# Kernel tuning notes

Measured on AMD Instinct MI355X. Metric: run time of the kernel, lower is better.

The kernel has to match this reference:

```python
import jax, jax.numpy as jnp
import numpy as np

NUM_HEADS = 16
CAUSAL = True


def setup_inputs() -> dict:
    key = jax.random.key(0)
    ks = jax.random.split(key, 3)
    B, T, D = 2, 2048, 1024
    s = 1.0 / np.sqrt(D)
    return {
        "x": jax.random.normal(ks[0], (B, T, D), dtype=jnp.float32),
        "W_qkv": jax.random.normal(ks[1], (3 * D, D), dtype=jnp.float32) * s,
        "b_qkv": jnp.zeros((3 * D,), dtype=jnp.float32),
        "W_out": jax.random.normal(ks[2], (D, D), dtype=jnp.float32) * s,
        "b_out": jnp.zeros((D,), dtype=jnp.float32),
    }


def reference(x, W_qkv, b_qkv, W_out, b_out):
    B, T, D = x.shape
    H = NUM_HEADS
    hd = D // H
    # qkv projection: torch Linear y = x @ W.T + b
    qkv = jnp.einsum('btd,ed->bte', x, W_qkv) + b_qkv  # [B,T,3D]
    qkv = qkv.reshape(B, T, H, 3 * hd).transpose(0, 2, 1, 3)  # [B,H,T,3hd]
    q, k, v = jnp.split(qkv, 3, axis=-1)  # each [B,H,T,hd]
    scale = 1.0 / np.sqrt(hd).astype(np.float32)
    scores = jnp.einsum('bhtd,bhsd->bhts', q, k) * scale  # [B,H,T,T]
    if CAUSAL:
        mask = jnp.triu(jnp.ones((T, T), dtype=bool), k=1)
        scores = jnp.where(mask, jnp.float32(-jnp.inf), scores)
    weights = jax.nn.softmax(scores, axis=-1)
    attn = jnp.einsum('bhts,bhsd->bhtd', weights, v)  # [B,H,T,hd]
    out = attn.transpose(0, 2, 1, 3).reshape(B, T, D)
    return jnp.einsum('btd,ed->bte', out, W_out) + b_out
```

## Files before the change

### kernel.cpp

```cpp
#include <hip/hip_runtime.h>
#include <hip/hip_bf16.h>
#include <cstdint>


using short8  = __attribute__((ext_vector_type(8))) short;
using floatx4 = __attribute__((ext_vector_type(4))) float;

#define LDS_STRIDE 40

__device__ __forceinline__ float bf16_to_f32(unsigned short u) {
    union { unsigned int i; float f; } v; v.i = ((unsigned int)u) << 16; return v.f;
}
__device__ __forceinline__ unsigned short f32_to_bf16(float f) {
    union { float f; unsigned int i; } v; v.f = f;
    unsigned int x = v.i;
    unsigned int r = x + 0x7FFFu + ((x >> 16) & 1u);
    return (unsigned short)(r >> 16);
}
__device__ __forceinline__ short8 cvt8(const float* __restrict__ p) {
    const float4 f0 = *(const float4*)p;
    const float4 f1 = *(const float4*)(p + 4);
    short8 r;
    r[0] = (short)f32_to_bf16(f0.x); r[1] = (short)f32_to_bf16(f0.y);
    r[2] = (short)f32_to_bf16(f0.z); r[3] = (short)f32_to_bf16(f0.w);
    r[4] = (short)f32_to_bf16(f1.x); r[5] = (short)f32_to_bf16(f1.y);
    r[6] = (short)f32_to_bf16(f1.z); r[7] = (short)f32_to_bf16(f1.w);
    return r;
}
__device__ __forceinline__ unsigned int cvtpk(float a, float b) {
    unsigned int r;
    asm("v_cvt_pk_bf16_f32 %0, %1, %2" : "=v"(r) : "v"(a), "v"(b));
    return r;
}

#define Q_PRESCALE 0.1803368801111204f

#if __has_builtin(__builtin_amdgcn_global_load_lds)
#define ASYNC_STAGE 1
typedef const __attribute__((address_space(1))) void* gas1_t;
typedef __attribute__((address_space(3))) void* las3_t;
#else
#define ASYNC_STAGE 0
#endif

__device__ __forceinline__ void gload_lds16(const ushort* g, ushort* l) {
#if ASYNC_STAGE
    __builtin_amdgcn_global_load_lds((gas1_t)g, (las3_t)l, 16, 0, 0);
#else
    *(short8*)l = *(const short8*)g;
#endif
}

__device__ __forceinline__ int v_slot(int k) {
    const int k5 = k & 31;
    return (k & 32) + ((k5 >> 4) & 1) * 4 + ((k5 >> 2) & 3) * 8 + (k5 & 3);
}

__global__ __launch_bounds__(256, 8) void cvt_bf16_3(
    const float* __restrict__ x,  const float* __restrict__ wq,
    const float* __restrict__ wo, ushort* __restrict__ xb,
    ushort* __restrict__ wqb, ushort* __restrict__ wob)
{
    const int i = blockIdx.x * 256 + threadIdx.x;
    const float* src; ushort* dst; int off;
    if (i < 524288)      { src = x;  dst = xb;  off = i; }
    else if (i < 917504) { src = wq; dst = wqb; off = i - 524288; }
    else                 { src = wo; dst = wob; off = i - 917504; }
    *(short8*)(dst + (size_t)off * 8) = cvt8(src + (size_t)off * 8);
}

__global__ __launch_bounds__(256, 3) void gemm_qkv(
    const ushort* __restrict__ A, const ushort* __restrict__ W,
    const float* __restrict__ bias,
    ushort* __restrict__ Cq, ushort* __restrict__ Ck, ushort* __restrict__ Cv,
    int M, int N, int K)
{
    __shared__ __align__(16) ushort As[128 * 64];
    __shared__ __align__(16) ushort Bs[128 * 64];

    const int tid  = threadIdx.x;
    const int lane = tid & 63;
    const int wave = tid >> 6;
    const int wm = (wave >> 1) * 64;
    const int wn = (wave & 1) * 64;
    const int m0 = blockIdx.x * 128;
    const int n0 = blockIdx.y * 128;
    const int quad = lane >> 4;
    const int l16  = lane & 15;

    floatx4 acc[4][4];
#pragma unroll
    for (int i = 0; i < 4; i++)
#pragma unroll
        for (int j = 0; j < 4; j++) acc[i][j] = (floatx4)0.0f;

    const int rb  = tid >> 3;
    const int lch = (tid & 7) ^ (rb & 7);
    const ushort* pA = A + (size_t)(m0 + rb) * K + lch * 8;
    const ushort* pB = W + (size_t)(n0 + rb) * K + lch * 8;
    const size_t cstep = (size_t)32 * K;

    const int Ra = wm + l16;
    const int aoff0 = Ra * 64 + ((quad       ^ (Ra & 7)) << 3);
    const int aoff1 = Ra * 64 + (((4 + quad) ^ (Ra & 7)) << 3);
    const int Rb = wn + l16;
    const int boff0 = Rb * 64 + ((quad       ^ (Rb & 7)) << 3);
    const int boff1 = Rb * 64 + (((4 + quad) ^ (Rb & 7)) << 3);

    for (int k0 = 0; k0 < K; k0 += 64) {
        __syncthreads();
#pragma unroll
        for (int c = 0; c < 4; c++) {
            gload_lds16(pA + c * cstep + k0, &As[c * 2048 + wave * 512]);
            gload_lds16(pB + c * cstep + k0, &Bs[c * 2048 + wave * 512]);
        }
        __syncthreads();

        short8 af0[4], af1[4];
#pragma unroll
        for (int i = 0; i < 4; i++) {
            af0[i] = *(const short8*)&As[aoff0 + i * 1024];
            af1[i] = *(const short8*)&As[aoff1 + i * 1024];
        }
#pragma unroll
        for (int j = 0; j < 4; j++) {
            const short8 bf0 = *(const short8*)&Bs[boff0 + j * 1024];
            const short8 bf1 = *(const short8*)&Bs[boff1 + j * 1024];
#pragma unroll
            for (int i = 0; i < 4; i++) {
                acc[i][j] = __builtin_amdgcn_mfma_f32_16x16x32_bf16(af0[i], bf0, acc[i][j], 0, 0, 0);
                acc[i][j] = __builtin_amdgcn_mfma_f32_16x16x32_bf16(af1[i], bf1, acc[i][j], 0, 0, 0);
            }
        }
    }

#pragma unroll
    for (int i = 0; i < 4; i++) {
#pragma unroll
        for (int j = 0; j < 4; j++) {
#pragma unroll
            for (int r = 0; r < 4; r++) {
                const int row = m0 + wm + i * 16 + quad * 4 + r;
                const int col = n0 + wn + j * 16 + l16;
                float v = acc[i][j][r] + bias[col];
                const int h  = col / 192;
                const int rr = col - h * 192;
                const int sel = rr >> 6;
                const int d   = rr & 63;
                const int b = row >> 11;
                const int t = row & 2047;
                const int bh = b * 16 + h;
                if (sel == 0) {
                    Cq[(((size_t)bh) * 2048 + t) * 64 + d] =
                        f32_to_bf16(v * Q_PRESCALE);
                } else if (sel == 1) {
                    Ck[(((size_t)bh) * 2048 + t) * 64 + d] = f32_to_bf16(v);
                } else {
                    Cv[(((size_t)bh * 32 + (t >> 6)) * 64 + d) * 64 + v_slot(t & 63)] =
                        f32_to_bf16(v);
                }
            }
        }
    }
}

__global__ __launch_bounds__(256, 3) void gemm_out(
    const ushort* __restrict__ A, const ushort* __restrict__ W,
    const float* __restrict__ bias, float* __restrict__ Cout,
    int M, int N, int K)
{
    __shared__ __align__(16) ushort As[128 * 64];
    __shared__ __align__(16) ushort Bs[64 * 64];

    const int tid  = threadIdx.x;
    const int lane = tid & 63;
    const int wave = tid >> 6;
    const int wm = (wave >> 1) * 64;
    const int wn = (wave & 1) * 32;
    const int m0 = blockIdx.x * 128;
    const int n0 = blockIdx.y * 64;
    const int quad = lane >> 4;
    const int l16  = lane & 15;

    floatx4 acc[4][2];
#pragma unroll
    for (int i = 0; i < 4; i++)
#pragma unroll
        for (int j = 0; j < 2; j++) acc[i][j] = (floatx4)0.0f;

    const int rb  = tid >> 3;
    const int lch = (tid & 7) ^ (rb & 7);
    const ushort* pA = A + (size_t)(m0 + rb) * K + lch * 8;
    const ushort* pB = W + (size_t)(n0 + rb) * K + lch * 8;
    const size_t cstep = (size_t)32 * K;

    const int Ra = wm + l16;
    const int aoff0 = Ra * 64 + ((quad       ^ (Ra & 7)) << 3);
    const int aoff1 = Ra * 64 + (((4 + quad) ^ (Ra & 7)) << 3);
    const int Rb = wn + l16;
    const int boff0 = Rb * 64 + ((quad       ^ (Rb & 7)) << 3);
    const int boff1 = Rb * 64 + (((4 + quad) ^ (Rb & 7)) << 3);

    for (int k0 = 0; k0 < K; k0 += 64) {
        __syncthreads();
#pragma unroll
        for (int c = 0; c < 4; c++)
            gload_lds16(pA + c * cstep + k0, &As[c * 2048 + wave * 512]);
#pragma unroll
        for (int c = 0; c < 2; c++)
            gload_lds16(pB + c * cstep + k0, &Bs[c * 2048 + wave * 512]);
        __syncthreads();

        short8 af0[4], af1[4];
#pragma unroll
        for (int i = 0; i < 4; i++) {
            af0[i] = *(const short8*)&As[aoff0 + i * 1024];
            af1[i] = *(const short8*)&As[aoff1 + i * 1024];
        }
#pragma unroll
        for (int j = 0; j < 2; j++) {
            const short8 bf0 = *(const short8*)&Bs[boff0 + j * 1024];
            const short8 bf1 = *(const short8*)&Bs[boff1 + j * 1024];
#pragma unroll
            for (int i = 0; i < 4; i++) {
                acc[i][j] = __builtin_amdgcn_mfma_f32_16x16x32_bf16(af0[i], bf0, acc[i][j], 0, 0, 0);
                acc[i][j] = __builtin_amdgcn_mfma_f32_16x16x32_bf16(af1[i], bf1, acc[i][j], 0, 0, 0);
            }
        }
    }

#pragma unroll
    for (int i = 0; i < 4; i++) {
#pragma unroll
        for (int j = 0; j < 2; j++) {
#pragma unroll
            for (int r = 0; r < 4; r++) {
                const int row = m0 + wm + i * 16 + quad * 4 + r;
                const int col = n0 + wn + j * 16 + l16;
                Cout[(size_t)row * N + col] = acc[i][j][r] + bias[col];
            }
        }
    }
}

template <int MODE, int AFP32>
__global__ __launch_bounds__(256, 2) void gemm_bt(
    const void* __restrict__ Av, const float* __restrict__ W,
    const float* __restrict__ bias,
    ushort* __restrict__ Cq, ushort* __restrict__ Ck, ushort* __restrict__ Cv,
    float* __restrict__ Cout, int M, int N, int K)
{
    __shared__ __align__(16) ushort As[128 * LDS_STRIDE];
    __shared__ __align__(16) ushort Bs[128 * LDS_STRIDE];

    const int tid  = threadIdx.x;
    const int lane = tid & 63;
    const int wave = tid >> 6;
    const int wm = (wave >> 1) * 64;
    const int wn = (wave & 1) * 64;
    const int m0 = blockIdx.x * 128;
    const int n0 = blockIdx.y * 128;
    const int quad = lane >> 4;
    const int l16  = lane & 15;

    floatx4 acc[4][4];
#pragma unroll
    for (int i = 0; i < 4; i++)
#pragma unroll
        for (int j = 0; j < 4; j++) acc[i][j] = (floatx4)0.0f;

    const int srow = tid >> 2;
    const int scol = (tid & 3) * 8;

    for (int k0 = 0; k0 < K; k0 += 32) {
        short8 a0, a1;
        if (AFP32) {
            const float* A = (const float*)Av;
            a0 = cvt8(A + (size_t)(m0 + srow) * K + k0 + scol);
            a1 = cvt8(A + (size_t)(m0 + srow + 64) * K + k0 + scol);
        } else {
            const ushort* A = (const ushort*)Av;
            a0 = *(const short8*)(A + (size_t)(m0 + srow) * K + k0 + scol);
            a1 = *(const short8*)(A + (size_t)(m0 + srow + 64) * K + k0 + scol);
        }
        const short8 b0 = cvt8(W + (size_t)(n0 + srow) * K + k0 + scol);
        const short8 b1 = cvt8(W + (size_t)(n0 + srow + 64) * K + k0 + scol);
        __syncthreads();
        *(short8*)&As[srow * LDS_STRIDE + scol] = a0;
        *(short8*)&As[(srow + 64) * LDS_STRIDE + scol] = a1;
        *(short8*)&Bs[srow * LDS_STRIDE + scol] = b0;
        *(short8*)&Bs[(srow + 64) * LDS_STRIDE + scol] = b1;
        __syncthreads();

        short8 af[4], bf[4];
#pragma unroll
        for (int i = 0; i < 4; i++)
            af[i] = *(const short8*)&As[(wm + i * 16 + l16) * LDS_STRIDE + quad * 8];
#pragma unroll
        for (int j = 0; j < 4; j++)
            bf[j] = *(const short8*)&Bs[(wn + j * 16 + l16) * LDS_STRIDE + quad * 8];
#pragma unroll
        for (int i = 0; i < 4; i++)
#pragma unroll
            for (int j = 0; j < 4; j++)
                acc[i][j] = __builtin_amdgcn_mfma_f32_16x16x32_bf16(af[i], bf[j], acc[i][j], 0, 0, 0);
    }

#pragma unroll
    for (int i = 0; i < 4; i++) {
#pragma unroll
        for (int j = 0; j < 4; j++) {
#pragma unroll
            for (int r = 0; r < 4; r++) {
                const int row = m0 + wm + i * 16 + quad * 4 + r;
                const int col = n0 + wn + j * 16 + l16;
                float v = acc[i][j][r] + bias[col];
                if (MODE == 0) {
                    const int h  = col / 192;
                    const int rr = col - h * 192;
                    const int sel = rr >> 6;
                    const int d   = rr & 63;
                    const int b = row >> 11;
                    const int t = row & 2047;
                    const int bh = b * 16 + h;
                    if (sel == 0) {
                        Cq[(((size_t)bh) * 2048 + t) * 64 + d] =
                            f32_to_bf16(v * Q_PRESCALE);
                    } else if (sel == 1) {
                        Ck[(((size_t)bh) * 2048 + t) * 64 + d] = f32_to_bf16(v);
                    } else {
                        Cv[(((size_t)bh * 32 + (t >> 6)) * 64 + d) * 64 + v_slot(t & 63)] =
                            f32_to_bf16(v);
                    }
                } else {
                    Cout[(size_t)row * N + col] = v;
                }
            }
        }
    }
}

__global__ __launch_bounds__(256, 4) void attn_mfma(
    const ushort* __restrict__ Q, const ushort* __restrict__ K,
    const ushort* __restrict__ Vtb, ushort* __restrict__ O)
{
    const int bid   = blockIdx.x;
    const int bh    = bid & 31;
    const int qtIdx = bid >> 5;
    const int qi    = (qtIdx < 16) ? (31 - qtIdx) : (qtIdx - 16);
    const int tid  = threadIdx.x;
    const int wave = tid >> 6;
    const int lane = tid & 63;
    const int quad = lane >> 4;
    const int l16  = lane & 15;
    const int qb   = qi * 64 + wave * 16;

    __shared__ __align__(16) ushort Ks[2][4096];
    __shared__ __align__(16) ushort Vs[2][4096];

    const size_t kbase = (size_t)bh * 2048 * 64;

    const int ob0 = tid * 16, ob1 = ob0 + 4096;
    const int r0 = ob0 >> 7, c0 = (ob0 >> 4) & 7;
    const int r1 = ob1 >> 7, c1 = (ob1 >> 4) & 7;
    const int e0 = r0 * 64 + ((c0 ^ (r0 & 7)) << 3);
    const int e1 = r1 * 64 + ((c1 ^ (r1 & 7)) << 3);
    const ushort* Kb = K + kbase;
    const ushort* Vb = Vtb + (size_t)bh * 32 * 4096;

    auto stage = [&](int t, ushort* KsB, ushort* VsB) {
        const ushort* Ktile = Kb + t * 4096;
        const ushort* Vtile = Vb + t * 4096;
        gload_lds16(Ktile + e0, KsB + wave * 512);
        gload_lds16(Ktile + e1, KsB + 2048 + wave * 512);
        gload_lds16(Vtile + e0, VsB + wave * 512);
        gload_lds16(Vtile + e1, VsB + 2048 + wave * 512);
    };

    const int sw0 = ((quad ^ (l16 & 7)) << 3);
    const int sw1 = (((4 + quad) ^ (l16 & 7)) << 3);
    const int rbase = l16 * 64;

    short8 qf0, qf1;
    {
        const ushort* qp = Q + kbase + (size_t)(qb + l16) * 64 + quad * 8;
        qf0 = *(const short8*)qp;
        qf1 = *(const short8*)(qp + 32);
    }

    floatx4 accO[4];
#pragma unroll
    for (int d = 0; d < 4; d++) accO[d] = (floatx4)0.0f;
    float accLs = 0.0f;

    union PB { unsigned int u[4]; short8 s8; };

    auto compute = [&](int t, const ushort* KsB, const ushort* VsB) {
        short8 kf[4][2];
#pragma unroll
        for (int j = 0; j < 4; j++) {
            kf[j][0] = *(const short8*)&KsB[j * 1024 + rbase + sw0];
            kf[j][1] = *(const short8*)&KsB[j * 1024 + rbase + sw1];
        }
        floatx4 sc[4];
#pragma unroll
        for (int j = 0; j < 4; j++) {
            floatx4 acc = (floatx4)0.0f;
            acc = __builtin_amdgcn_mfma_f32_16x16x32_bf16(kf[j][0], qf0, acc, 0, 0, 0);
            acc = __builtin_amdgcn_mfma_f32_16x16x32_bf16(kf[j][1], qf1, acc, 0, 0, 0);
            sc[j] = acc;
        }
        if (t * 64 + 63 > qb) {
            const int qcol = qb + l16;
#pragma unroll
            for (int j = 0; j < 4; j++) {
                const int keyb = t * 64 + j * 16 + quad * 4;
#pragma unroll
                for (int r = 0; r < 4; r++)
                    if (keyb + r > qcol) sc[j][r] = -1e30f;
            }
        }
#pragma unroll
        for (int j = 0; j < 4; j++)
#pragma unroll
            for (int r = 0; r < 4; r++)
                sc[j][r] = __builtin_amdgcn_exp2f(sc[j][r]);
        const floatx4 ssum = sc[0] + sc[1] + sc[2] + sc[3];
        accLs += (ssum[0] + ssum[1]) + (ssum[2] + ssum[3]);
        PB p0, p1;
#pragma unroll
        for (int j = 0; j < 2; j++) {
            p0.u[j * 2 + 0] = cvtpk(sc[j][0], sc[j][1]);
            p0.u[j * 2 + 1] = cvtpk(sc[j][2], sc[j][3]);
            p1.u[j * 2 + 0] = cvtpk(sc[j + 2][0], sc[j + 2][1]);
            p1.u[j * 2 + 1] = cvtpk(sc[j + 2][2], sc[j + 2][3]);
        }
        short8 vf[4][2];
#pragma unroll
        for (int d = 0; d < 4; d++) {
            vf[d][0] = *(const short8*)&VsB[d * 1024 + rbase + sw0];
            vf[d][1] = *(const short8*)&VsB[d * 1024 + rbase + sw1];
        }
#pragma unroll
        for (int d = 0; d < 4; d++) {
            accO[d] = __builtin_amdgcn_mfma_f32_16x16x32_bf16(p0.s8, vf[d][0], accO[d], 0, 0, 0);
            accO[d] = __builtin_amdgcn_mfma_f32_16x16x32_bf16(p1.s8, vf[d][1], accO[d], 0, 0, 0);
        }
    };

    const int nt = qi + 1;
    stage(0, Ks[0], Vs[0]);
    __syncthreads();
    int t = 0;
    while (true) {
        if (t + 1 < nt) stage(t + 1, Ks[1], Vs[1]);
        compute(t, Ks[0], Vs[0]);
        __syncthreads();
        if (++t >= nt) break;
        if (t + 1 < nt) stage(t + 1, Ks[0], Vs[0]);
        compute(t, Ks[1], Vs[1]);
        __syncthreads();
        if (++t >= nt) break;
    }

    const int b = bh >> 4, h = bh & 15;
    {
        float L = accLs;
        L += __shfl_xor(L, 16);
        L += __shfl_xor(L, 32);
        float inv[4];
#pragma unroll
        for (int r = 0; r < 4; r++) inv[r] = 1.0f / __shfl(L, quad * 4 + r);
#pragma unroll
        for (int d = 0; d < 4; d++)
#pragma unroll
            for (int r = 0; r < 4; r++)
                O[(size_t)(b * 2048 + qb + quad * 4 + r) * 1024 + h * 64 + d * 16 + l16] =
                    f32_to_bf16(accO[d][r] * inv[r]);
    }
}

extern "C" void kernel_launch(void* const* d_in, const int* in_sizes, int n_in,
                              void* d_out, int out_size, void* d_ws, size_t ws_size,
                              hipStream_t stream) {
    const float* x    = (const float*)d_in[0];
    const float* Wqkv = (const float*)d_in[1];
    const float* bqkv = (const float*)d_in[2];
    const float* Wout = (const float*)d_in[3];
    const float* bout = (const float*)d_in[4];
    float* out = (float*)d_out;

    char* ws = (char*)d_ws;
    const size_t MB = 1024 * 1024;
    ushort* Q    = (ushort*)(ws + 0 * MB);
    ushort* Kk   = (ushort*)(ws + 8 * MB);
    ushort* Vtb  = (ushort*)(ws + 16 * MB);
    ushort* O    = (ushort*)(ws + 24 * MB);

    const dim3 blk(256);
    if (ws_size >= 48 * MB) {
        ushort* xb    = (ushort*)(ws + 32 * MB);
        ushort* Wqkvb = (ushort*)(ws + 40 * MB);
        ushort* Woutb = (ushort*)(ws + 46 * MB);
        cvt_bf16_3<<<dim3(4096), blk, 0, stream>>>(x, Wqkv, Wout, xb, Wqkvb, Woutb);
        gemm_qkv<<<dim3(32, 24), blk, 0, stream>>>(xb, Wqkvb, bqkv, Q, Kk, Vtb,
                                                   4096, 3072, 1024);
        attn_mfma<<<dim3(1024), blk, 0, stream>>>(Q, Kk, Vtb, O);
        gemm_out<<<dim3(32, 16), blk, 0, stream>>>(O, Woutb, bout, out,
                                                   4096, 1024, 1024);
    } else {
        gemm_bt<0, 1><<<dim3(32, 24), blk, 0, stream>>>(x, Wqkv, bqkv, Q, Kk, Vtb,
                                                        nullptr, 4096, 3072, 1024);
        attn_mfma<<<dim3(1024), blk, 0, stream>>>(Q, Kk, Vtb, O);
        gemm_bt<1, 0><<<dim3(32, 8), blk, 0, stream>>>(O, Wout, bout, nullptr, nullptr,
                                                       nullptr, out, 4096, 1024, 1024);
    }
}
```

Baseline: 164.4 us.

## Give each wave private LDS tiles with optional async double-buffered staging in QKV GEMM

Restructures the QKV projection GEMM so each wave stages its own 64-row A and B slices into a private LDS region at a K step of 32, using a new swizzled fragment layout. Under ASYNC_STAGE it double-buffers with vmcnt-based waits instead of block barriers, so loads overlap MFMA work. The aim is to drop block-wide synchronisation and overlap memory with compute. In exchange, wave pairs re-fetch the same global tiles, LDS use grows enough that the occupancy hint drops from 3 to 2, and the non-async fallback adds more barrier-separated iterations.

```diff
diff --git a/kernel.cpp b/kernel.cpp
--- a/kernel.cpp
+++ b/kernel.cpp
@@ -69,14 +69,13 @@
     *(short8*)(dst + (size_t)off * 8) = cvt8(src + (size_t)off * 8);
 }
 
-__global__ __launch_bounds__(256, 3) void gemm_qkv(
+__global__ __launch_bounds__(256, 2) void gemm_qkv(
     const ushort* __restrict__ A, const ushort* __restrict__ W,
     const float* __restrict__ bias,
     ushort* __restrict__ Cq, ushort* __restrict__ Ck, ushort* __restrict__ Cv,
     int M, int N, int K)
 {
-    __shared__ __align__(16) ushort As[128 * 64];
-    __shared__ __align__(16) ushort Bs[128 * 64];
+    __shared__ __align__(16) ushort S[4][8192];
 
     const int tid  = threadIdx.x;
     const int lane = tid & 63;
@@ -87,6 +86,7 @@
     const int n0 = blockIdx.y * 128;
     const int quad = lane >> 4;
     const int l16  = lane & 15;
+    ushort* Sw = &S[wave][0];
 
     floatx4 acc[4][4];
 #pragma unroll
@@ -94,45 +94,70 @@
 #pragma unroll
         for (int j = 0; j < 4; j++) acc[i][j] = (floatx4)0.0f;
 
-    const int rb  = tid >> 3;
-    const int lch = (tid & 7) ^ (rb & 7);
-    const ushort* pA = A + (size_t)(m0 + rb) * K + lch * 8;
-    const ushort* pB = W + (size_t)(n0 + rb) * K + lch * 8;
-    const size_t cstep = (size_t)32 * K;
-
-    const int Ra = wm + l16;
-    const int aoff0 = Ra * 64 + ((quad       ^ (Ra & 7)) << 3);
-    const int aoff1 = Ra * 64 + (((4 + quad) ^ (Ra & 7)) << 3);
-    const int Rb = wn + l16;
-    const int boff0 = Rb * 64 + ((quad       ^ (Rb & 7)) << 3);
-    const int boff1 = Rb * 64 + (((4 + quad) ^ (Rb & 7)) << 3);
-
-    for (int k0 = 0; k0 < K; k0 += 64) {
-        __syncthreads();
-#pragma unroll
-        for (int c = 0; c < 4; c++) {
-            gload_lds16(pA + c * cstep + k0, &As[c * 2048 + wave * 512]);
-            gload_lds16(pB + c * cstep + k0, &Bs[c * 2048 + wave * 512]);
-        }
-        __syncthreads();
-
-        short8 af0[4], af1[4];
-#pragma unroll
-        for (int i = 0; i < 4; i++) {
-            af0[i] = *(const short8*)&As[aoff0 + i * 1024];
-            af1[i] = *(const short8*)&As[aoff1 + i * 1024];
-        }
-#pragma unroll
-        for (int j = 0; j < 4; j++) {
-            const short8 bf0 = *(const short8*)&Bs[boff0 + j * 1024];
-            const short8 bf1 = *(const short8*)&Bs[boff1 + j * 1024];
-#pragma unroll
-            for (int i = 0; i < 4; i++) {
-                acc[i][j] = __builtin_amdgcn_mfma_f32_16x16x32_bf16(af0[i], bf0, acc[i][j], 0, 0, 0);
-                acc[i][j] = __builtin_amdgcn_mfma_f32_16x16x32_bf16(af1[i], bf1, acc[i][j], 0, 0, 0);
-            }
-        }
-    }
+    const ushort* pA[4];
+    const ushort* pB[4];
+#pragma unroll
+    for (int p = 0; p < 4; p++) {
+        const int ob   = lane * 16 + p * 1024;
+        const int line = ob >> 7;
+        const int pp   = ((ob >> 4) & 7) ^ (line & 7);
+        const int row  = line * 2 + (pp >> 2);
+        const int ch   = pp & 3;
+        pA[p] = A + (size_t)(m0 + wm + row) * K + ch * 8;
+        pB[p] = W + (size_t)(n0 + wn + row) * K + ch * 8;
+    }
+
+    auto stage = [&](int k0, int buf) {
+        ushort* da = Sw + buf * 2048;
+        ushort* db = Sw + 4096 + buf * 2048;
+#pragma unroll
+        for (int p = 0; p < 4; p++) {
+            gload_lds16(pA[p] + k0, da + p * 512);
+            gload_lds16(pB[p] + k0, db + p * 512);
+        }
+    };
+
+    const int foff = (l16 >> 1) * 64 +
+                     (((((l16 & 1) << 2) + quad) ^ ((l16 >> 1) & 7)) << 3);
+
+    auto compute = [&](int buf) {
+        const ushort* a = Sw + buf * 2048;
+        const ushort* b = Sw + 4096 + buf * 2048;
+        short8 af[4], bf[4];
+#pragma unroll
+        for (int i = 0; i < 4; i++) af[i] = *(const short8*)&a[foff + i * 512];
+#pragma unroll
+        for (int j = 0; j < 4; j++) bf[j] = *(const short8*)&b[foff + j * 512];
+#pragma unroll
+        for (int i = 0; i < 4; i++)
+#pragma unroll
+            for (int j = 0; j < 4; j++)
+                acc[i][j] = __builtin_amdgcn_mfma_f32_16x16x32_bf16(af[i], bf[j], acc[i][j], 0, 0, 0);
+    };
+
+#if ASYNC_STAGE
+    const int NT = K >> 5;
+    stage(0, 0);
+    stage(32, 1);
+    int buf = 0;
+    for (int t = 0; t < NT; ++t) {
+        if (t + 1 < NT) {
+            asm volatile("s_waitcnt vmcnt(8)" ::: "memory");
+        } else {
+            asm volatile("s_waitcnt vmcnt(0)" ::: "memory");
+        }
+        compute(buf);
+        if (t + 2 < NT) stage((t + 2) * 32, buf);
+        buf ^= 1;
+    }
+#else
+    for (int k0 = 0; k0 < K; k0 += 32) {
+        stage(k0, 0);
+        __syncthreads();
+        compute(0);
+        __syncthreads();
+    }
+#endif
 
 #pragma unroll
     for (int i = 0; i < 4; i++) {
```

Measured after the change: 175.6 us. 1.07x slower.
